# Kernel tuning notes

Measured on AMD Instinct MI355X. Metric: run time of the kernel, lower is better.

The kernel has to match this reference:

```python
import jax, jax.numpy as jnp
import numpy as np

VAR0, VAR1 = 0.1, 0.2          # SSD variances
IOU_THRESH = 0.5
NUM_CLASSES = 21
NEGPOS_RATIO = 3
ALPHA = 1.0


def mid_to_corner(b):
    # [cx,cy,w,h] -> [xmin,ymin,xmax,ymax]
    return jnp.concatenate([b[:, :2] - b[:, 2:] / 2, b[:, :2] + b[:, 2:] / 2], axis=1)


def jaccard(box_a, box_b):
    # box_a [n,4], box_b [P,4] corner form -> IoU [n,P]
    lt = jnp.maximum(box_a[:, None, :2], box_b[None, :, :2])
    rb = jnp.minimum(box_a[:, None, 2:], box_b[None, :, 2:])
    wh = jnp.clip(rb - lt, 0.0)
    inter = wh[..., 0] * wh[..., 1]
    area_a = (box_a[:, 2] - box_a[:, 0]) * (box_a[:, 3] - box_a[:, 1])
    area_b = (box_b[:, 2] - box_b[:, 0]) * (box_b[:, 3] - box_b[:, 1])
    union = area_a[:, None] + area_b[None, :] - inter
    return inter / union


def encode_offset(matched, priors):
    # matched corner form [P,4], priors center form [P,4]
    g_cxcy = ((matched[:, :2] + matched[:, 2:]) / 2 - priors[:, :2]) / (VAR0 * priors[:, 2:])
    g_wh = jnp.log((matched[:, 2:] - matched[:, :2]) / priors[:, 2:]) / VAR1
    return jnp.concatenate([g_cxcy, g_wh], axis=1)


def match_one(gt_box, gt_cls, valid, priors_corner, priors_mid):
    # gt_box [n,4], gt_cls [n], valid [n] bool; priors [P,4]
    n = gt_box.shape[0]
    P = priors_corner.shape[0]
    ovl = jaccard(gt_box, priors_corner)                    # [n,P]
    ovl = jnp.where(valid[:, None], ovl, -1.0)              # mask padded GTs
    best_truth_idx = jnp.argmax(ovl, axis=0)                # [P]
    best_truth_ovl = jnp.max(ovl, axis=0)                   # [P]
    best_prior_idx = jnp.argmax(ovl, axis=1)                # [n]
    bpi = jnp.where(valid, best_prior_idx, P)               # OOB for padded -> dropped
    best_truth_ovl = best_truth_ovl.at[bpi].set(2.0, mode='drop')
    best_truth_idx = best_truth_idx.at[bpi].set(jnp.arange(n), mode='drop')
    matches = gt_box[best_truth_idx]                        # [P,4]
    loc = encode_offset(matches, priors_mid)                # [P,4]
    conf = gt_cls[best_truth_idx].astype(jnp.int32) + 1     # [P]
    conf = jnp.where(best_truth_ovl < IOU_THRESH, 0, conf)
    return loc, conf


def setup_inputs() -> dict:
    key = jax.random.key(0)
    k = jax.random.split(key, 8)
    B, P, C, NMAX = 64, 8732, 21, 50
    confidence = jax.random.normal(k[0], (B, P, C), dtype=jnp.float32)
    location = 0.1 * jax.random.normal(k[1], (B, P, 4), dtype=jnp.float32)
    cxcy = jax.random.uniform(k[2], (P, 2), minval=0.05, maxval=0.95)
    pwh = jax.random.uniform(k[3], (P, 2), minval=0.05, maxval=0.4)
    prior_boxes = jnp.concatenate([cxcy, pwh], axis=1).astype(jnp.float32)
    xymin = jax.random.uniform(k[4], (B, NMAX, 2), minval=0.0, maxval=0.6)
    gwh = jax.random.uniform(k[5], (B, NMAX, 2), minval=0.05, maxval=0.35)
    cls = jax.random.randint(k[6], (B, NMAX), 0, C - 1).astype(jnp.float32)
    labels = jnp.concatenate([xymin, xymin + gwh, cls[..., None]], axis=-1).astype(jnp.float32)
    obj_count = jax.random.randint(k[7], (B, 1), 1, NMAX + 1).astype(jnp.int32)
    return {"confidence": confidence, "location": location,
            "prior_boxes": prior_boxes, "labels": labels, "obj_count": obj_count}


def reference(confidence, location, prior_boxes, labels, obj_count):
    B, P, C = confidence.shape
    NMAX = labels.shape[1]
    priors_corner = mid_to_corner(prior_boxes)
    valid = jnp.arange(NMAX)[None, :] < obj_count            # [B,NMAX]
    loc_t, conf_t = jax.vmap(match_one, in_axes=(0, 0, 0, None, None))(
        labels[..., :4], labels[..., 4], valid, priors_corner, prior_boxes)
    # loc_t [B,P,4] float, conf_t [B,P] int32

    pos = conf_t > 0                                          # [B,P]
    # smooth-L1 over positive anchors (sum reduction)
    d = jnp.abs(location - loc_t)
    sl1 = jnp.where(d < 1.0, 0.5 * d * d, d - 0.5)
    loss_loc = jnp.sum(sl1 * pos[..., None].astype(sl1.dtype))

    # hard negative mining score: global-max logsumexp minus target logit
    bc = confidence.reshape(-1, C)
    x_max = jnp.max(bc)
    lse = jnp.log(jnp.sum(jnp.exp(bc - x_max), axis=1)) + x_max
    tgt_logit = jnp.take_along_axis(bc, conf_t.reshape(-1, 1), axis=1)[:, 0]
    loss_c = (lse - tgt_logit).reshape(B, P)
    loss_c = jnp.where(pos, 0.0, loss_c)
    loss_idx = jnp.argsort(-loss_c, axis=1)                   # descending sort
    idx_rank = jnp.argsort(loss_idx, axis=1)
    num_pos = jnp.sum(pos.astype(jnp.int32), axis=1, keepdims=True)   # [B,1]
    num_neg = jnp.clip(NEGPOS_RATIO * num_pos, None, P - 1)
    neg = idx_rank < num_neg                                  # [B,P]

    # standard cross entropy over selected (pos|neg) anchors, sum reduction
    logp = jax.nn.log_softmax(confidence, axis=-1)            # [B,P,C]
    nll = -jnp.take_along_axis(logp, conf_t[..., None], axis=-1)[..., 0]
    sel = jnp.logical_or(pos, neg)
    loss_conf = jnp.sum(nll * sel.astype(nll.dtype))

    N = jnp.sum(num_pos).astype(confidence.dtype)
    return (ALPHA * loss_loc / N, loss_conf / N)
```

## Files before the change

kernel.cpp:

```cpp
#include <hip/hip_runtime.h>
#include <math.h>

#define Bn 64
#define Pn 8732
#define Cn 21
#define NMAXn 50
#define PX 35
#define Wn 16

__global__ __launch_bounds__(256) void k_bpp(const float* __restrict__ labels,
                                             const int* __restrict__ objc,
                                             const float* __restrict__ priors,
                                             int* __restrict__ match,
                                             unsigned long long* __restrict__ slot) {
    const int b = blockIdx.y;
    const int px = blockIdx.x;
    const int tid = threadIdx.x;
    __shared__ float4 lab4[NMAXn];
    __shared__ float gaa[NMAXn];
    __shared__ float qm[NMAXn][257];
    __shared__ int cnt_s;
    if (tid == 0) cnt_s = objc[b];
    __syncthreads();
    const int cnt = cnt_s;
    if (tid < cnt) {
        const float* lb = labels + (b * NMAXn + tid) * 5;
        const float x0 = lb[0], y0 = lb[1], x1 = lb[2], y1 = lb[3];
        lab4[tid] = make_float4(x0, y0, x1, y1);
        gaa[tid] = (x1 - x0) * (y1 - y0);
    }
    __syncthreads();

    const int p = px * 256 + tid;
    const bool valid = p < Pn;
    const int pcl = valid ? p : (Pn - 1);
    const float4 pr = reinterpret_cast<const float4*>(priors)[pcl];
    const float px0 = pr.x - 0.5f * pr.z, py0 = pr.y - 0.5f * pr.w;
    const float px1 = pr.x + 0.5f * pr.z, py1 = pr.y + 0.5f * pr.w;
    const float parea = (px1 - px0) * (py1 - py0);
    float best = -1.0f;
    int bidx = 0;
    for (int n = 0; n < cnt; ++n) {
        const float4 g = lab4[n];
        const float ga = gaa[n];
        const float lx = fmaxf(g.x, px0), ly = fmaxf(g.y, py0);
        const float rx = fminf(g.z, px1), ry = fminf(g.w, py1);
        const float w = fmaxf(rx - lx, 0.0f), h = fmaxf(ry - ly, 0.0f);
        const float inter = w * h;
        float q = inter / (ga + parea - inter);
        if (!valid) q = -2.0f;
        qm[n][tid] = q;
        if (q > best) { best = q; bidx = n; }
    }
    if (valid) match[(size_t)b * Pn + p] = (bidx << 1) | (best >= 0.5f ? 1 : 0);
    __syncthreads();

    const int n = tid >> 2, sub = tid & 3;
    if (n < cnt) {
        const int base = sub * 64;
        float bq = -3.0f;
        int bj = base;
        for (int j = 0; j < 64; ++j) {
            const float q = qm[n][base + j];
            if (q > bq) { bq = q; bj = base + j; }
        }
#pragma unroll
        for (int off = 2; off > 0; off >>= 1) {
            const float oq = __shfl_down(bq, off);
            const int oj = __shfl_down(bj, off);
            if (oq > bq || (oq == bq && oj < bj)) { bq = oq; bj = oj; }
        }
        if (sub == 0) {
            const unsigned gp = (unsigned)(px * 256 + bj);
            const unsigned long long key =
                ((unsigned long long)__float_as_uint(bq) << 32) |
                (unsigned long long)(0xFFFFFFFFu - gp);
            atomicMax(&slot[b * NMAXn + n], key);
        }
    }
}

__global__ __launch_bounds__(64) void k_bpr(const int* __restrict__ objc,
                                            const unsigned long long* __restrict__ slot,
                                            int* __restrict__ match,
                                            int* __restrict__ done) {
    __shared__ int sbp[NMAXn];
    const int b = blockIdx.x;
    const int tid = threadIdx.x;
    if (b == 0 && tid == 0) *done = 0;
    const int cnt = objc[b];
    if (tid < cnt) {
        const unsigned long long key = slot[b * NMAXn + tid];
        sbp[tid] = (int)(0xFFFFFFFFu - (unsigned)(key & 0xFFFFFFFFull));
    }
    __syncthreads();
    if (tid < cnt) {
        const int myp = sbp[tid];
        bool win = true;
        for (int n2 = tid + 1; n2 < cnt; ++n2) win = win && (sbp[n2] != myp);
        if (win) match[(size_t)b * Pn + myp] = (tid << 1) | 1;
    }
}

__global__ __launch_bounds__(256) void k_main(const float* __restrict__ conf,
                                              const float* __restrict__ loc,
                                              const float* __restrict__ priors,
                                              const float* __restrict__ labels,
                                              const int* __restrict__ match,
                                              float* __restrict__ lc,
                                              float* __restrict__ part_loc,
                                              float* __restrict__ part_nll,
                                              int* __restrict__ part_np) {
    const int b = blockIdx.y;
    const int px = blockIdx.x;
    const int p0 = px * 256;
    const int tid = threadIdx.x;
    const int rows = min(256, Pn - p0);
    const int p = p0 + ((tid < rows) ? tid : 0);
    const size_t gi = (size_t)b * Pn + p;
    const int w = match[gi];

    __shared__ float sconf[256 * Cn];
    __shared__ float lab[NMAXn * 5];
    const float4* src = reinterpret_cast<const float4*>(conf + ((size_t)b * Pn + p0) * Cn);
    const int n4 = rows * Cn / 4;
    for (int i = tid; i < n4; i += 256) reinterpret_cast<float4*>(sconf)[i] = src[i];
    for (int i = tid; i < NMAXn * 5; i += 256) lab[i] = labels[b * NMAXn * 5 + i];
    __syncthreads();

    float my_loc = 0.0f, my_nll = 0.0f;
    int my_np = 0;
    if (tid < rows) {
        const int ti = w >> 1;
        const int ct = (w & 1) ? ((int)lab[ti * 5 + 4] + 1) : 0;
        const float* row = sconf + tid * Cn;
        float m = row[0];
#pragma unroll
        for (int j = 1; j < Cn; ++j) m = fmaxf(m, row[j]);
        float s2 = 0.0f;
#pragma unroll
        for (int j = 0; j < Cn; ++j) s2 += __expf(row[j] - m);
        const float nll = __logf(s2) + m - row[ct];
        if (ct > 0) {
            lc[gi] = 0.0f;
            my_np = 1;
            my_nll = nll;
            const float4 pr = reinterpret_cast<const float4*>(priors)[p];
            const float gx0 = lab[ti * 5 + 0], gy0 = lab[ti * 5 + 1];
            const float gx1 = lab[ti * 5 + 2], gy1 = lab[ti * 5 + 3];
            const float tx = ((gx0 + gx1) * 0.5f - pr.x) / (0.1f * pr.z);
            const float ty = ((gy0 + gy1) * 0.5f - pr.y) / (0.1f * pr.w);
            const float tw = __logf((gx1 - gx0) / pr.z) * 5.0f;
            const float th = __logf((gy1 - gy0) / pr.w) * 5.0f;
            const float4 l = reinterpret_cast<const float4*>(loc)[gi];
            float d;
            d = fabsf(l.x - tx); my_loc += (d < 1.0f) ? 0.5f * d * d : d - 0.5f;
            d = fabsf(l.y - ty); my_loc += (d < 1.0f) ? 0.5f * d * d : d - 0.5f;
            d = fabsf(l.z - tw); my_loc += (d < 1.0f) ? 0.5f * d * d : d - 0.5f;
            d = fabsf(l.w - th); my_loc += (d < 1.0f) ? 0.5f * d * d : d - 0.5f;
        } else {
            lc[gi] = nll;
        }
    }
    for (int off = 32; off > 0; off >>= 1) {
        my_loc += __shfl_down(my_loc, off);
        my_nll += __shfl_down(my_nll, off);
        my_np += __shfl_down(my_np, off);
    }
    __shared__ float rl[4], rn[4];
    __shared__ int rp[4];
    const int wid = tid >> 6, lane = tid & 63;
    if (lane == 0) { rl[wid] = my_loc; rn[wid] = my_nll; rp[wid] = my_np; }
    __syncthreads();
    if (tid == 0) {
        const int g = b * PX + px;
        part_loc[g] = rl[0] + rl[1] + rl[2] + rl[3];
        part_nll[g] = rn[0] + rn[1] + rn[2] + rn[3];
        part_np[g] = rp[0] + rp[1] + rp[2] + rp[3];
    }
}

__global__ __launch_bounds__(1024) void k_neg(const float* __restrict__ lc,
                                              const float* __restrict__ part_loc,
                                              const float* __restrict__ part_nll,
                                              const int* __restrict__ part_np,
                                              float* __restrict__ negsum,
                                              int* __restrict__ done,
                                              float* __restrict__ out) {
    const int b = blockIdx.x;
    const int tid = threadIdx.x;
    const int lane = tid & 63, wid = tid >> 6;
    __shared__ int redc[2][Wn];
    __shared__ float redf[Wn], redf2[Wn];
    __shared__ int redi[Wn];
    __shared__ int np_sh, islast;

    const int NV = Pn / 4;
    const float4* src = reinterpret_cast<const float4*>(lc + (size_t)b * Pn);
    const float4 sent = make_float4(-1.0f, -1.0f, -1.0f, -1.0f);
    float4 r0 = (tid < NV) ? src[tid] : sent;
    float4 r1 = (tid + 1024 < NV) ? src[tid + 1024] : sent;
    float4 r2 = (tid + 2048 < NV) ? src[tid + 2048] : sent;

    if (tid < 64) {
        int npl = (tid < PX) ? part_np[b * PX + tid] : 0;
        for (int off = 32; off > 0; off >>= 1) npl += __shfl_down(npl, off);
        if (tid == 0) np_sh = npl;
    }
    __syncthreads();
    const int k = min(3 * np_sh, Pn - 1);

    unsigned lo = 0u, hi = 0x7F800000u;
#pragma unroll 1
    for (int it = 0; it < 31; ++it) {
        const unsigned mid = lo + ((hi - lo) >> 1);
        const float fm = __uint_as_float(mid);
        int c = (r0.x >= fm) + (r0.y >= fm) + (r0.z >= fm) + (r0.w >= fm)
              + (r1.x >= fm) + (r1.y >= fm) + (r1.z >= fm) + (r1.w >= fm)
              + (r2.x >= fm) + (r2.y >= fm) + (r2.z >= fm) + (r2.w >= fm);
        for (int off = 32; off > 0; off >>= 1) c += __shfl_down(c, off);
        if (lane == 0) redc[it & 1][wid] = c;
        __syncthreads();
        int tot = 0;
#pragma unroll
        for (int w = 0; w < Wn; ++w) tot += redc[it & 1][w];
        if (tot >= k) lo = mid;
        else hi = mid;
    }
    const float v = __uint_as_float(lo);

    float sm = 0.0f;
    int c = 0;
    if (r0.x > v) { sm += r0.x; ++c; }
    if (r0.y > v) { sm += r0.y; ++c; }
    if (r0.z > v) { sm += r0.z; ++c; }
    if (r0.w > v) { sm += r0.w; ++c; }
    if (r1.x > v) { sm += r1.x; ++c; }
    if (r1.y > v) { sm += r1.y; ++c; }
    if (r1.z > v) { sm += r1.z; ++c; }
    if (r1.w > v) { sm += r1.w; ++c; }
    if (r2.x > v) { sm += r2.x; ++c; }
    if (r2.y > v) { sm += r2.y; ++c; }
    if (r2.z > v) { sm += r2.z; ++c; }
    if (r2.w > v) { sm += r2.w; ++c; }
    for (int off = 32; off > 0; off >>= 1) {
        sm += __shfl_down(sm, off);
        c += __shfl_down(c, off);
    }
    if (lane == 0) { redf[wid] = sm; redi[wid] = c; }
    __syncthreads();
    if (tid == 0) {
        float st = 0.0f;
        int ct = 0;
#pragma unroll
        for (int w = 0; w < Wn; ++w) { st += redf[w]; ct += redi[w]; }
        negsum[b] = st + (float)(k - ct) * v;
        __threadfence();
        islast = (atomicAdd(done, 1) == Bn - 1) ? 1 : 0;
    }
    __syncthreads();
    if (!islast) return;
    __threadfence();

    float sl = 0.0f, sn = 0.0f;
    int np = 0;
    for (int i = tid; i < Bn * PX; i += 1024) {
        sl += part_loc[i];
        sn += part_nll[i];
        np += part_np[i];
    }
    if (tid < Bn) sn += negsum[tid];
    for (int off = 32; off > 0; off >>= 1) {
        sl += __shfl_down(sl, off);
        sn += __shfl_down(sn, off);
        np += __shfl_down(np, off);
    }
    if (lane == 0) { redf[wid] = sn; redf2[wid] = sl; redi[wid] = np; }
    __syncthreads();
    if (tid == 0) {
        float tsl = 0.0f, tsn = 0.0f;
        int tnp = 0;
#pragma unroll
        for (int w = 0; w < Wn; ++w) { tsl += redf2[w]; tsn += redf[w]; tnp += redi[w]; }
        const float fN = (float)tnp;
        out[0] = tsl / fN;
        out[1] = tsn / fN;
    }
}

extern "C" void kernel_launch(void* const* d_in, const int* in_sizes, int n_in,
                              void* d_out, int out_size, void* d_ws, size_t ws_size,
                              hipStream_t stream) {
    const float* conf = (const float*)d_in[0];
    const float* loc = (const float*)d_in[1];
    const float* priors = (const float*)d_in[2];
    const float* labels = (const float*)d_in[3];
    const int* objc = (const int*)d_in[4];
    float* out = (float*)d_out;

    unsigned long long* slot = (unsigned long long*)d_ws;
    float* part_loc = (float*)((char*)d_ws + 25600);
    float* part_nll = part_loc + Bn * PX;
    int* part_np = (int*)(part_nll + Bn * PX);
    float* negsum = (float*)(part_np + Bn * PX);
    int* match = (int*)(negsum + Bn);
    float* lc = (float*)(match + (size_t)Bn * Pn);
    int* done = (int*)(lc + (size_t)Bn * Pn);

    hipMemsetAsync(slot, 0, Bn * NMAXn * sizeof(unsigned long long), stream);

    dim3 g(PX, Bn);
    k_bpp<<<g, 256, 0, stream>>>(labels, objc, priors, match, slot);
    k_bpr<<<Bn, 64, 0, stream>>>(objc, slot, match, done);
    k_main<<<g, 256, 0, stream>>>(conf, loc, priors, labels, match, lc,
                                  part_loc, part_nll, part_np);
    k_neg<<<Bn, 1024, 0, stream>>>(lc, part_loc, part_nll, part_np, negsum, done, out);
}
```

Baseline: 81.37 us.

## Replace shared-memory IoU argmax and atomics with per-wave DPP reductions and partial keys

In the matching kernel, the shared IoU matrix and its atomicMax slots are replaced by a wave-level DPP max plus ballot for each ground truth. Each wave writes a partial key, and the bipartite-resolve kernel scans those 140 keys per GT, so the memset and atomics go away. The main kernel loads each confidence row straight into registers instead of staging it through shared memory. All shuffle reductions become DPP row and broadcast reductions. The trade-offs are a serial reduction per GT inside the inner loop, 140 global reads per GT in the resolve kernel, and strided per-thread row loads that lose coalescing.

```diff
diff --git a/kernel.cpp b/kernel.cpp
--- a/kernel.cpp
+++ b/kernel.cpp
@@ -8,28 +8,45 @@
 #define PX 35
 #define Wn 16
 
+template <int C>
+__device__ __forceinline__ float dppf(float x) {
+    return __int_as_float(__builtin_amdgcn_update_dpp(0, __float_as_int(x), C, 0xf, 0xf, true));
+}
+template <int C>
+__device__ __forceinline__ int dppi(int x) {
+    return __builtin_amdgcn_update_dpp(0, x, C, 0xf, 0xf, true);
+}
+__device__ __forceinline__ float wave_max_f(float x) {
+    x = fmaxf(x, dppf<0x111>(x));
+    x = fmaxf(x, dppf<0x112>(x));
+    x = fmaxf(x, dppf<0x114>(x));
+    x = fmaxf(x, dppf<0x118>(x));
+    x = fmaxf(x, dppf<0x142>(x));
+    x = fmaxf(x, dppf<0x143>(x));
+    return x;
+}
+__device__ __forceinline__ float wave_sum_f(float x) {
+    x += dppf<0x111>(x); x += dppf<0x112>(x); x += dppf<0x114>(x);
+    x += dppf<0x118>(x); x += dppf<0x142>(x); x += dppf<0x143>(x);
+    return x;
+}
+__device__ __forceinline__ int wave_sum_i(int x) {
+    x += dppi<0x111>(x); x += dppi<0x112>(x); x += dppi<0x114>(x);
+    x += dppi<0x118>(x); x += dppi<0x142>(x); x += dppi<0x143>(x);
+    return x;
+}
+
 __global__ __launch_bounds__(256) void k_bpp(const float* __restrict__ labels,
                                              const int* __restrict__ objc,
                                              const float* __restrict__ priors,
                                              int* __restrict__ match,
-                                             unsigned long long* __restrict__ slot) {
+                                             unsigned long long* __restrict__ bpk) {
     const int b = blockIdx.y;
     const int px = blockIdx.x;
     const int tid = threadIdx.x;
-    __shared__ float4 lab4[NMAXn];
-    __shared__ float gaa[NMAXn];
-    __shared__ float qm[NMAXn][257];
-    __shared__ int cnt_s;
-    if (tid == 0) cnt_s = objc[b];
-    __syncthreads();
-    const int cnt = cnt_s;
-    if (tid < cnt) {
-        const float* lb = labels + (b * NMAXn + tid) * 5;
-        const float x0 = lb[0], y0 = lb[1], x1 = lb[2], y1 = lb[3];
-        lab4[tid] = make_float4(x0, y0, x1, y1);
-        gaa[tid] = (x1 - x0) * (y1 - y0);
-    }
-    __syncthreads();
+    const int lane = tid & 63, wid = tid >> 6;
+    const int cnt = objc[b];
+    const float* lb = labels + b * NMAXn * 5;
 
     const int p = px * 256 + tid;
     const bool valid = p < Pn;
@@ -38,50 +55,37 @@
     const float px0 = pr.x - 0.5f * pr.z, py0 = pr.y - 0.5f * pr.w;
     const float px1 = pr.x + 0.5f * pr.z, py1 = pr.y + 0.5f * pr.w;
     const float parea = (px1 - px0) * (py1 - py0);
+
     float best = -1.0f;
     int bidx = 0;
     for (int n = 0; n < cnt; ++n) {
-        const float4 g = lab4[n];
-        const float ga = gaa[n];
-        const float lx = fmaxf(g.x, px0), ly = fmaxf(g.y, py0);
-        const float rx = fminf(g.z, px1), ry = fminf(g.w, py1);
+        const float gx0 = lb[n * 5 + 0], gy0 = lb[n * 5 + 1];
+        const float gx1 = lb[n * 5 + 2], gy1 = lb[n * 5 + 3];
+        const float lx = fmaxf(gx0, px0), ly = fmaxf(gy0, py0);
+        const float rx = fminf(gx1, px1), ry = fminf(gy1, py1);
         const float w = fmaxf(rx - lx, 0.0f), h = fmaxf(ry - ly, 0.0f);
         const float inter = w * h;
-        float q = inter / (ga + parea - inter);
-        if (!valid) q = -2.0f;
-        qm[n][tid] = q;
+        const float ga = (gx1 - gx0) * (gy1 - gy0);
+        const float q = inter / (ga + parea - inter);
         if (q > best) { best = q; bidx = n; }
+        const float qr = valid ? q : 0.0f;
+        const float m = wave_max_f(qr);
+        const float s_q = __int_as_float(__builtin_amdgcn_readlane(__float_as_int(m), 63));
+        const unsigned long long mask = __ballot(qr == s_q);
+        const int first = __ffsll(mask) - 1;
+        if (lane == 0) {
+            const int pw = px * 256 + (wid << 6) + first;
+            const unsigned long long key =
+                ((unsigned long long)__float_as_uint(s_q) << 32) |
+                (unsigned long long)(65535 - pw);
+            bpk[(size_t)(b * NMAXn + n) * (PX * 4) + px * 4 + wid] = key;
+        }
     }
     if (valid) match[(size_t)b * Pn + p] = (bidx << 1) | (best >= 0.5f ? 1 : 0);
-    __syncthreads();
-
-    const int n = tid >> 2, sub = tid & 3;
-    if (n < cnt) {
-        const int base = sub * 64;
-        float bq = -3.0f;
-        int bj = base;
-        for (int j = 0; j < 64; ++j) {
-            const float q = qm[n][base + j];
-            if (q > bq) { bq = q; bj = base + j; }
-        }
-#pragma unroll
-        for (int off = 2; off > 0; off >>= 1) {
-            const float oq = __shfl_down(bq, off);
-            const int oj = __shfl_down(bj, off);
-            if (oq > bq || (oq == bq && oj < bj)) { bq = oq; bj = oj; }
-        }
-        if (sub == 0) {
-            const unsigned gp = (unsigned)(px * 256 + bj);
-            const unsigned long long key =
-                ((unsigned long long)__float_as_uint(bq) << 32) |
-                (unsigned long long)(0xFFFFFFFFu - gp);
-            atomicMax(&slot[b * NMAXn + n], key);
-        }
-    }
 }
 
 __global__ __launch_bounds__(64) void k_bpr(const int* __restrict__ objc,
-                                            const unsigned long long* __restrict__ slot,
+                                            const unsigned long long* __restrict__ bpk,
                                             int* __restrict__ match,
                                             int* __restrict__ done) {
     __shared__ int sbp[NMAXn];
@@ -90,8 +94,13 @@
     if (b == 0 && tid == 0) *done = 0;
     const int cnt = objc[b];
     if (tid < cnt) {
-        const unsigned long long key = slot[b * NMAXn + tid];
-        sbp[tid] = (int)(0xFFFFFFFFu - (unsigned)(key & 0xFFFFFFFFull));
+        const size_t g0 = (size_t)(b * NMAXn + tid) * (PX * 4);
+        unsigned long long best = 0ull;
+        for (int t = 0; t < PX * 4; ++t) {
+            const unsigned long long k = bpk[g0 + t];
+            best = (k > best) ? k : best;
+        }
+        sbp[tid] = 65535 - (int)(best & 0xFFFFull);
     }
     __syncthreads();
     if (tid < cnt) {
@@ -120,34 +129,34 @@
     const size_t gi = (size_t)b * Pn + p;
     const int w = match[gi];
 
-    __shared__ float sconf[256 * Cn];
-    __shared__ float lab[NMAXn * 5];
-    const float4* src = reinterpret_cast<const float4*>(conf + ((size_t)b * Pn + p0) * Cn);
-    const int n4 = rows * Cn / 4;
-    for (int i = tid; i < n4; i += 256) reinterpret_cast<float4*>(sconf)[i] = src[i];
-    for (int i = tid; i < NMAXn * 5; i += 256) lab[i] = labels[b * NMAXn * 5 + i];
-    __syncthreads();
+    const float* row = conf + gi * Cn;
+    float a[Cn];
+#pragma unroll
+    for (int j = 0; j < Cn; ++j) a[j] = row[j];
 
     float my_loc = 0.0f, my_nll = 0.0f;
     int my_np = 0;
     if (tid < rows) {
         const int ti = w >> 1;
-        const int ct = (w & 1) ? ((int)lab[ti * 5 + 4] + 1) : 0;
-        const float* row = sconf + tid * Cn;
-        float m = row[0];
-#pragma unroll
-        for (int j = 1; j < Cn; ++j) m = fmaxf(m, row[j]);
+        int ct = 0;
+        if (w & 1) ct = (int)labels[(b * NMAXn + ti) * 5 + 4] + 1;
+        float m = a[0];
+#pragma unroll
+        for (int j = 1; j < Cn; ++j) m = fmaxf(m, a[j]);
         float s2 = 0.0f;
 #pragma unroll
-        for (int j = 0; j < Cn; ++j) s2 += __expf(row[j] - m);
-        const float nll = __logf(s2) + m - row[ct];
+        for (int j = 0; j < Cn; ++j) s2 += __expf(a[j] - m);
+        float tgt = a[0];
+#pragma unroll
+        for (int j = 1; j < Cn; ++j) tgt = (ct == j) ? a[j] : tgt;
+        const float nll = __logf(s2) + m - tgt;
         if (ct > 0) {
             lc[gi] = 0.0f;
             my_np = 1;
             my_nll = nll;
+            const float* lbp = labels + (b * NMAXn + ti) * 5;
+            const float gx0 = lbp[0], gy0 = lbp[1], gx1 = lbp[2], gy1 = lbp[3];
             const float4 pr = reinterpret_cast<const float4*>(priors)[p];
-            const float gx0 = lab[ti * 5 + 0], gy0 = lab[ti * 5 + 1];
-            const float gx1 = lab[ti * 5 + 2], gy1 = lab[ti * 5 + 3];
             const float tx = ((gx0 + gx1) * 0.5f - pr.x) / (0.1f * pr.z);
             const float ty = ((gy0 + gy1) * 0.5f - pr.y) / (0.1f * pr.w);
             const float tw = __logf((gx1 - gx0) / pr.z) * 5.0f;
@@ -162,15 +171,13 @@
             lc[gi] = nll;
         }
     }
-    for (int off = 32; off > 0; off >>= 1) {
-        my_loc += __shfl_down(my_loc, off);
-        my_nll += __shfl_down(my_nll, off);
-        my_np += __shfl_down(my_np, off);
-    }
+    my_loc = wave_sum_f(my_loc);
+    my_nll = wave_sum_f(my_nll);
+    my_np = wave_sum_i(my_np);
     __shared__ float rl[4], rn[4];
     __shared__ int rp[4];
     const int wid = tid >> 6, lane = tid & 63;
-    if (lane == 0) { rl[wid] = my_loc; rn[wid] = my_nll; rp[wid] = my_np; }
+    if (lane == 63) { rl[wid] = my_loc; rn[wid] = my_nll; rp[wid] = my_np; }
     __syncthreads();
     if (tid == 0) {
         const int g = b * PX + px;
@@ -204,8 +211,8 @@
 
     if (tid < 64) {
         int npl = (tid < PX) ? part_np[b * PX + tid] : 0;
-        for (int off = 32; off > 0; off >>= 1) npl += __shfl_down(npl, off);
-        if (tid == 0) np_sh = npl;
+        npl = wave_sum_i(npl);
+        if (tid == 63) np_sh = npl;
     }
     __syncthreads();
     const int k = min(3 * np_sh, Pn - 1);
@@ -218,8 +225,8 @@
         int c = (r0.x >= fm) + (r0.y >= fm) + (r0.z >= fm) + (r0.w >= fm)
               + (r1.x >= fm) + (r1.y >= fm) + (r1.z >= fm) + (r1.w >= fm)
               + (r2.x >= fm) + (r2.y >= fm) + (r2.z >= fm) + (r2.w >= fm);
-        for (int off = 32; off > 0; off >>= 1) c += __shfl_down(c, off);
-        if (lane == 0) redc[it & 1][wid] = c;
+        c = wave_sum_i(c);
+        if (lane == 63) redc[it & 1][wid] = c;
         __syncthreads();
         int tot = 0;
 #pragma unroll
@@ -243,11 +250,9 @@
     if (r2.y > v) { sm += r2.y; ++c; }
     if (r2.z > v) { sm += r2.z; ++c; }
     if (r2.w > v) { sm += r2.w; ++c; }
-    for (int off = 32; off > 0; off >>= 1) {
-        sm += __shfl_down(sm, off);
-        c += __shfl_down(c, off);
-    }
-    if (lane == 0) { redf[wid] = sm; redi[wid] = c; }
+    sm = wave_sum_f(sm);
+    c = wave_sum_i(c);
+    if (lane == 63) { redf[wid] = sm; redi[wid] = c; }
     __syncthreads();
     if (tid == 0) {
         float st = 0.0f;
@@ -270,12 +275,10 @@
         np += part_np[i];
     }
     if (tid < Bn) sn += negsum[tid];
-    for (int off = 32; off > 0; off >>= 1) {
-        sl += __shfl_down(sl, off);
-        sn += __shfl_down(sn, off);
-        np += __shfl_down(np, off);
-    }
-    if (lane == 0) { redf[wid] = sn; redf2[wid] = sl; redi[wid] = np; }
+    sl = wave_sum_f(sl);
+    sn = wave_sum_f(sn);
+    np = wave_sum_i(np);
+    if (lane == 63) { redf[wid] = sn; redf2[wid] = sl; redi[wid] = np; }
     __syncthreads();
     if (tid == 0) {
         float tsl = 0.0f, tsn = 0.0f;
@@ -298,8 +301,8 @@
     const int* objc = (const int*)d_in[4];
     float* out = (float*)d_out;
 
-    unsigned long long* slot = (unsigned long long*)d_ws;
-    float* part_loc = (float*)((char*)d_ws + 25600);
+    unsigned long long* bpk = (unsigned long long*)d_ws;
+    float* part_loc = (float*)(bpk + (size_t)Bn * NMAXn * PX * 4);
     float* part_nll = part_loc + Bn * PX;
     int* part_np = (int*)(part_nll + Bn * PX);
     float* negsum = (float*)(part_np + Bn * PX);
@@ -307,11 +310,9 @@
     float* lc = (float*)(match + (size_t)Bn * Pn);
     int* done = (int*)(lc + (size_t)Bn * Pn);
 
-    hipMemsetAsync(slot, 0, Bn * NMAXn * sizeof(unsigned long long), stream);
-
     dim3 g(PX, Bn);
-    k_bpp<<<g, 256, 0, stream>>>(labels, objc, priors, match, slot);
-    k_bpr<<<Bn, 64, 0, stream>>>(objc, slot, match, done);
+    k_bpp<<<g, 256, 0, stream>>>(labels, objc, priors, match, bpk);
+    k_bpr<<<Bn, 64, 0, stream>>>(objc, bpk, match, done);
     k_main<<<g, 256, 0, stream>>>(conf, loc, priors, labels, match, lc,
                                   part_loc, part_nll, part_np);
     k_neg<<<Bn, 1024, 0, stream>>>(lc, part_loc, part_nll, part_np, negsum, done, out);
```

Measured after the change: 78.65 us. -3.3%, faster.
